# Performance work log

Hardware: AMD Instinct MI355X
Metric: run time of the kernel (lower is better)

The kernel has to match this reference:

```python
import jax, jax.numpy as jnp
import numpy as np

D = 512      # hidden_size
H = 8        # num_heads
EPS = 1e-5   # torch LayerNorm default eps


def _ln(x, g, b):
    m = x.mean(-1, keepdims=True)
    v = ((x - m) ** 2).mean(-1, keepdims=True)
    return (x - m) * jax.lax.rsqrt(v + EPS) * g + b


def _xavier(k, shape):
    fan_in, fan_out = shape
    lim = (6.0 / (fan_in + fan_out)) ** 0.5
    return jax.random.uniform(k, shape, jnp.float32, -lim, lim)


def setup_inputs() -> dict:
    key = jax.random.key(0)
    ks = jax.random.split(key, 8)
    lengths = np.array([512, 640, 768, 896, 1024, 512, 768, 1024], dtype=np.int64)
    cum = np.concatenate([np.zeros(1, np.int64), np.cumsum(lengths)])  # [9], last = 6144
    T = int(cum[-1])
    return {
        "h_n": jax.random.normal(ks[0], (T, D), jnp.float32),
        "to_v_w": _xavier(ks[1], (D, D)), "to_v_b": jnp.zeros((D,), jnp.float32),
        "to_qk_w": _xavier(ks[2], (D, 2 * D)), "to_qk_b": jnp.zeros((2 * D,), jnp.float32),
        "proj_w": _xavier(ks[3], (D, D)), "proj_b": jnp.zeros((D,), jnp.float32),
        "ffn_w1": _xavier(ks[4], (D, 4 * D)), "ffn_b1": jnp.zeros((4 * D,), jnp.float32),
        "ffn_w2": _xavier(ks[5], (4 * D, D)), "ffn_b2": jnp.zeros((D,), jnp.float32),
        "ln1_g": jnp.ones((D,), jnp.float32), "ln1_b": jnp.zeros((D,), jnp.float32),
        "ln2_g": jnp.ones((D,), jnp.float32), "ln2_b": jnp.zeros((D,), jnp.float32),
        "num_query_cumsum": jnp.asarray(cum),
    }


def reference(h_n, to_v_w, to_v_b, to_qk_w, to_qk_b, proj_w, proj_b,
              ffn_w1, ffn_b1, ffn_w2, ffn_b2, ln1_g, ln1_b, ln2_g, ln2_b,
              num_query_cumsum):
    # --- static ragged layout (indices are constants) ---
    cum = np.asarray(num_query_cumsum)
    lengths = np.diff(cum)                       # [B]
    B = int(lengths.size)
    N = int(lengths.max())                       # max_num_nodes
    T = int(cum[-1])
    bid = np.repeat(np.arange(B), lengths)       # [T] graph id per token
    pos = np.arange(T) - cum[bid]                # [T] slot within graph
    pad_mask = np.arange(N)[None, :] >= lengths[:, None]  # [B, N], True = padding

    hd = D // H
    scale = hd ** -0.5

    # --- projections on the flat ragged tokens ---
    v = h_n @ to_v_w + to_v_b                    # [T, D]
    qk = h_n @ to_qk_w + to_qk_b                 # [T, 2D]
    q, k = qk[:, :D], qk[:, D:]

    # --- pad ragged -> dense [B, H, N, hd] ---
    def pad(x):
        xp = jnp.zeros((B, N, D), x.dtype).at[bid, pos].set(x)
        return xp.reshape(B, N, H, hd).transpose(0, 2, 1, 3)

    qp, kp, vp = pad(q), pad(k), pad(v)

    # --- dense masked softmax attention (keys masked at pad slots) ---
    scores = jnp.einsum('bhnd,bhmd->bhnm', qp, kp) * scale
    scores = jnp.where(pad_mask[:, None, None, :], -jnp.inf, scores)
    attn = jax.nn.softmax(scores, axis=-1)
    ctx = jnp.einsum('bhnm,bhmd->bhnd', attn, vp)

    # --- unpad back to flat [T, D] ---
    h_new = ctx.transpose(0, 2, 1, 3).reshape(B, N, D)[bid, pos]

    # --- residual + LN + FFN + LN (dropout = 0) ---
    h1 = _ln(h_n + (h_new @ proj_w + proj_b), ln1_g, ln1_b)
    ffn = jax.nn.gelu(h1 @ ffn_w1 + ffn_b1, approximate=False) @ ffn_w2 + ffn_b2
    return _ln(h1 + ffn, ln2_g, ln2_b)
```

## Files before the change

### kernel.cpp

```cpp
#include <hip/hip_runtime.h>

typedef __bf16 bf16;
typedef __bf16 bf16x8 __attribute__((ext_vector_type(8)));
typedef __bf16 bf16x4 __attribute__((ext_vector_type(4)));
typedef float  f32x4  __attribute__((ext_vector_type(4)));

#define MFMA16 __builtin_amdgcn_mfma_f32_16x16x32_bf16

__device__ __forceinline__ void gl2lds16(const bf16* g, bf16* l) {
  __builtin_amdgcn_global_load_lds(
      (const __attribute__((address_space(1))) unsigned int*)g,
      (__attribute__((address_space(3))) unsigned int*)l, 16, 0, 0);
}

__device__ __forceinline__ int dt_bf16(const void* g1) {
  return (((const unsigned*)g1)[0] == 0x3F800000u) ? 0 : 1;
}
__device__ __forceinline__ float load_any(const void* p, int i, int f) {
  return f ? (float)((const bf16*)p)[i] : ((const float*)p)[i];
}

__device__ __forceinline__ float gelu_fast(float x) {
  const float u = 0.7978845608028654f * (x + 0.044715f * x * x * x);
  const float e = __builtin_amdgcn_exp2f(2.8853900817779268f * u);
  return x * e * __builtin_amdgcn_rcpf(e + 1.0f);
}

__global__ __launch_bounds__(256) void prep_all(
    const void* __restrict__ h, const void* __restrict__ w_qk,
    const void* __restrict__ w_v, const void* __restrict__ w_pr,
    const void* __restrict__ w_f1, const void* __restrict__ w_f2,
    const void* __restrict__ b_qk, const void* __restrict__ b_v,
    const void* __restrict__ b_pr, const void* __restrict__ b_f1,
    const void* __restrict__ b_f2, const void* __restrict__ g1,
    const void* __restrict__ b1, const void* __restrict__ g2,
    const void* __restrict__ b2,
    bf16* __restrict__ hb, bf16* __restrict__ Wtqkv, bf16* __restrict__ Wtpr,
    bf16* __restrict__ Wtf1, bf16* __restrict__ Wtf2,
    float* __restrict__ vec, int T) {
  __shared__ bf16 tile[32][33];
  const int f = dt_bf16(g1);
  const int t = threadIdx.x;
  int b = blockIdx.x;
  const int HB = (T * 512) / 2048;

  if (b < HB) {
    const int i = (b * 256 + t) * 8;
    if (f) {
      *(bf16x8*)&hb[i] = *(const bf16x8*)((const bf16*)h + i);
    } else {
      const float* hf = (const float*)h;
      bf16x8 v;
#pragma unroll
      for (int j = 0; j < 8; j++) v[j] = (bf16)hf[i + j];
      *(bf16x8*)&hb[i] = v;
    }
    return;
  }
  b -= HB;

  if (b < 3072) {
    const void* in; bf16* out; int K, N;
    if (b < 512)       { in = w_qk; out = Wtqkv;                     K = 512;  N = 1024; }
    else if (b < 768)  { b -= 512;  in = w_v;  out = Wtqkv + (size_t)1024 * 512; K = 512; N = 512; }
    else if (b < 1024) { b -= 768;  in = w_pr; out = Wtpr;           K = 512;  N = 512; }
    else if (b < 2048) { b -= 1024; in = w_f1; out = Wtf1;           K = 512;  N = 2048; }
    else               { b -= 2048; in = w_f2; out = Wtf2;           K = 2048; N = 512; }
    const int tilesx = N / 32;
    const int bx = (b % tilesx) * 32, by = (b / tilesx) * 32;
    const int tx = t & 31, ty = t >> 5;
#pragma unroll
    for (int i = 0; i < 32; i += 8)
      tile[ty + i][tx] = (bf16)load_any(in, (by + ty + i) * N + bx + tx, f);
    __syncthreads();
#pragma unroll
    for (int i = 0; i < 32; i += 8)
      out[(size_t)(bx + ty + i) * K + by + tx] = tile[tx][ty + i];
    return;
  }
  b -= 3072;

  const int i = b * 256 + t;
  if (i >= 6656) return;
  const void* src; int base;
  if (i < 1024)      { src = b_qk; base = 0; }
  else if (i < 1536) { src = b_v;  base = 1024; }
  else if (i < 2048) { src = b_pr; base = 1536; }
  else if (i < 4096) { src = b_f1; base = 2048; }
  else if (i < 4608) { src = b_f2; base = 4096; }
  else if (i < 5120) { src = g1;   base = 4608; }
  else if (i < 5632) { src = b1;   base = 5120; }
  else if (i < 6144) { src = g2;   base = 5632; }
  else               { src = b2;   base = 6144; }
  vec[i] = load_any(src, i - base, f);
}

template <int BM, int BN, int WM, int WN, int MODE>
__global__ __launch_bounds__(256) void gemm_lds(const bf16* __restrict__ A,
                                                const bf16* __restrict__ Bt,
                                                const float* __restrict__ bias,
                                                void* __restrict__ aux,
                                                void* __restrict__ outp,
                                                int N, int K, int ldA, int ldB,
                                                int ldT) {
  constexpr int WAVES_M = BM / WM;
  constexpr int WAVES_N = BN / WN;
  static_assert(WAVES_M * WAVES_N == 4, "4 waves per block");
  constexpr int MI = WM / 16;
  constexpr int NI = WN / 16;
  __shared__ __align__(16) bf16 As[BM * 64];
  __shared__ __align__(16) bf16 Bs[BN * 64];
  const int t = threadIdx.x;
  const int m0 = blockIdx.x * BM, n0 = blockIdx.y * BN;
  const int lane = t & 63, wv = t >> 6;
  const int wm = (wv / WAVES_N) * WM;
  const int wn = (wv % WAVES_N) * WN;
  const int qd = lane >> 4, cl = lane & 15;

  const f32x4 fz = {0.f, 0.f, 0.f, 0.f};
  f32x4 acc[MI][NI];
#pragma unroll
  for (int i = 0; i < MI; i++)
#pragma unroll
    for (int j = 0; j < NI; j++) acc[i][j] = fz;

  const int srow = wv * 8 + (lane >> 3);
  const int sch = (lane & 7) ^ (lane >> 3);
  const bf16* pA = A + (size_t)(m0 + srow) * ldA + sch * 8;
  const bf16* pB = Bt + (size_t)(n0 + srow) * ldB + sch * 8;
  bf16* AsW = As + wv * 8 * 64;
  bf16* BsW = Bs + wv * 8 * 64;

  for (int k0 = 0; k0 < K; k0 += 64) {
    __syncthreads();
#pragma unroll
    for (int op = 0; op < BM / 32; op++)
      gl2lds16(pA + (size_t)(op * 32) * ldA, AsW + op * 32 * 64);
#pragma unroll
    for (int op = 0; op < BN / 32; op++)
      gl2lds16(pB + (size_t)(op * 32) * ldB, BsW + op * 32 * 64);
    pA += 64; pB += 64;
    __syncthreads();

#pragma unroll
    for (int ss = 0; ss < 2; ss++) {
      bf16x8 af[MI], bfr[NI];
#pragma unroll
      for (int i = 0; i < MI; i++)
        af[i] = *(const bf16x8*)&As[(wm + i * 16 + cl) * 64 +
                                    ((ss * 4 + qd) ^ (cl & 7)) * 8];
#pragma unroll
      for (int i = 0; i < NI; i++)
        bfr[i] = *(const bf16x8*)&Bs[(wn + i * 16 + cl) * 64 +
                                     ((ss * 4 + qd) ^ (cl & 7)) * 8];
#pragma unroll
      for (int mi = 0; mi < MI; mi++)
#pragma unroll
        for (int ni = 0; ni < NI; ni++)
          acc[mi][ni] = MFMA16(af[mi], bfr[ni], acc[mi][ni], 0, 0, 0);
    }
  }

  float bv[NI];
#pragma unroll
  for (int ni = 0; ni < NI; ni++) bv[ni] = bias[n0 + wn + ni * 16 + cl];

#pragma unroll
  for (int mi = 0; mi < MI; mi++) {
    const int mbase = m0 + wm + mi * 16 + qd * 4;
#pragma unroll
    for (int ni = 0; ni < NI; ni++) {
      const int n = n0 + wn + ni * 16 + cl;
      if (MODE == 5) {
        if (n0 < 1024) {
          bf16* out = (bf16*)outp;
#pragma unroll
          for (int r = 0; r < 4; r++)
            out[(size_t)(mbase + r) * 1024 + n] = (bf16)(acc[mi][ni][r] + bv[ni]);
        } else {
          bf16* vtp = (bf16*)aux;
          bf16x4 pk;
#pragma unroll
          for (int r = 0; r < 4; r++) pk[r] = (bf16)(acc[mi][ni][r] + bv[ni]);
          *(bf16x4*)&vtp[(size_t)(n - 1024) * ldT + mbase] = pk;
        }
      } else if (MODE == 2) {
        float* out = (float*)outp;
        const bf16* res = (const bf16*)aux;
#pragma unroll
        for (int r = 0; r < 4; r++)
          out[(size_t)(mbase + r) * N + n] =
              acc[mi][ni][r] + bv[ni] + (float)res[(size_t)(mbase + r) * N + n];
      } else {
        bf16* out = (bf16*)outp;
#pragma unroll
        for (int r = 0; r < 4; r++)
          out[(size_t)(mbase + r) * N + n] = (bf16)gelu_fast(acc[mi][ni][r] + bv[ni]);
      }
    }
  }
}

__global__ __launch_bounds__(256) void attn_kernel(const bf16* __restrict__ qk,
                                                   const bf16* __restrict__ vt,
                                                   bf16* __restrict__ ctx,
                                                   const int* __restrict__ cumraw,
                                                   int T, int ncum) {
  __shared__ __align__(16) bf16 Ks[2][64 * 64];
  __shared__ __align__(16) bf16 Vs[2][64 * 64];
  __shared__ __align__(16) bf16 P[4][16 * 64];
  const int wv = threadIdx.x >> 6, lane = threadIdx.x & 63;
  const int qd = lane >> 4, cl = lane & 15;
  const int q0b = blockIdx.x * 64;
  const int q0 = q0b + wv * 16;
  const int h = blockIdx.y;

  const int stride = (cumraw[1] == 0) ? 2 : 1;
  int kstart = 0, kend = T;
  for (int i = 1; i < ncum; i++) {
    int c = cumraw[i * stride];
    if (c > q0b) { kend = c; break; }
    kstart = c;
  }

  const bf16* qbase = qk + (size_t)(q0 + cl) * 1024 + h * 64 + qd * 8;
  bf16x8 qf0 = *(const bf16x8*)qbase;
  bf16x8 qf1 = *(const bf16x8*)(qbase + 32);

  const f32x4 fz = {0.f, 0.f, 0.f, 0.f};
  f32x4 o[4] = {fz, fz, fz, fz};
  float lacc[4] = {0.f, 0.f, 0.f, 0.f};

  const int srow = wv * 8 + (lane >> 3);
  const int schunk = (lane & 7) ^ (srow & 7);
  const bf16* kg = qk + 512 + (size_t)h * 64 + schunk * 8;
  const bf16* vg = vt + (size_t)(h * 64 + srow) * T + schunk * 8;
  const int woff = wv * 8 * 64;

  const int bch = qd ^ (cl & 7);
  const float cc = 0.1803368801111204f;

  {
    const bf16* kg0 = kg + (size_t)(kstart + srow) * 1024;
    gl2lds16(kg0, Ks[0] + woff);
    gl2lds16(kg0 + (size_t)32 * 1024, Ks[0] + woff + 32 * 64);
    const bf16* vg0 = vg + kstart;
    gl2lds16(vg0, Vs[0] + woff);
    gl2lds16(vg0 + (size_t)32 * T, Vs[0] + woff + 32 * 64);
  }

  int ib = 0;
  for (int kc = kstart; kc < kend; kc += 64, ib ^= 1) {
    __syncthreads();

    if (kc + 64 < kend) {
      const bf16* kg0 = kg + (size_t)(kc + 64 + srow) * 1024;
      gl2lds16(kg0, Ks[ib ^ 1] + woff);
      gl2lds16(kg0 + (size_t)32 * 1024, Ks[ib ^ 1] + woff + 32 * 64);
      const bf16* vg0 = vg + kc + 64;
      gl2lds16(vg0, Vs[ib ^ 1] + woff);
      gl2lds16(vg0 + (size_t)32 * T, Vs[ib ^ 1] + woff + 32 * 64);
    }

    f32x4 s[4];
#pragma unroll
    for (int ni = 0; ni < 4; ni++) {
      const bf16* kr = Ks[ib] + (ni * 16 + cl) * 64;
      f32x4 tacc = fz;
      tacc = MFMA16(qf0, *(const bf16x8*)(kr + bch * 8), tacc, 0, 0, 0);
      tacc = MFMA16(qf1, *(const bf16x8*)(kr + (bch ^ 4) * 8), tacc, 0, 0, 0);
      s[ni] = tacc;
    }

    bf16* Pw = P[wv];
#pragma unroll
    for (int r = 0; r < 4; r++) {
      const float p0 = __builtin_amdgcn_exp2f(s[0][r] * cc);
      const float p1 = __builtin_amdgcn_exp2f(s[1][r] * cc);
      const float p2 = __builtin_amdgcn_exp2f(s[2][r] * cc);
      const float p3 = __builtin_amdgcn_exp2f(s[3][r] * cc);
      lacc[r] += (p0 + p1) + (p2 + p3);
      const int prow = qd * 4 + r;
      const int px = prow & 7;
      const int cb = cl >> 3, ci = cl & 7;
      Pw[prow * 64 + ((cb ^ px) * 8) + ci] = (bf16)p0;
      Pw[prow * 64 + (((2 + cb) ^ px) * 8) + ci] = (bf16)p1;
      Pw[prow * 64 + (((4 + cb) ^ px) * 8) + ci] = (bf16)p2;
      Pw[prow * 64 + (((6 + cb) ^ px) * 8) + ci] = (bf16)p3;
    }

    const int pch = qd ^ (cl & 7);
    const bf16* pr = Pw + cl * 64;
    bf16x8 pf0 = *(const bf16x8*)(pr + pch * 8);
    bf16x8 pf1 = *(const bf16x8*)(pr + (pch ^ 4) * 8);
#pragma unroll
    for (int dt = 0; dt < 4; dt++) {
      const bf16* vr = Vs[ib] + (dt * 16 + cl) * 64;
      o[dt] = MFMA16(pf0, *(const bf16x8*)(vr + bch * 8), o[dt], 0, 0, 0);
      o[dt] = MFMA16(pf1, *(const bf16x8*)(vr + (bch ^ 4) * 8), o[dt], 0, 0, 0);
    }
  }

  float linv[4];
#pragma unroll
  for (int r = 0; r < 4; r++) {
    float l = lacc[r];
    l += __shfl_xor(l, 1);
    l += __shfl_xor(l, 2);
    l += __shfl_xor(l, 4);
    l += __shfl_xor(l, 8);
    linv[r] = __builtin_amdgcn_rcpf(l);
  }
#pragma unroll
  for (int dt = 0; dt < 4; dt++) {
#pragma unroll
    for (int r = 0; r < 4; r++) {
      float y = o[dt][r] * linv[r];
      ctx[(size_t)(q0 + qd * 4 + r) * 512 + h * 64 + dt * 16 + cl] = (bf16)y;
    }
  }
}

__global__ __launch_bounds__(256) void ln_kernel(const float* __restrict__ s,
                                                 const float* __restrict__ g,
                                                 const float* __restrict__ b,
                                                 bf16* __restrict__ outb) {
  const int row = blockIdx.x * 4 + (threadIdx.x >> 6);
  const int lane = threadIdx.x & 63;
  const float4* sr = (const float4*)(s + (size_t)row * 512);
  float4 x0 = sr[lane];
  float4 x1 = sr[lane + 64];
  float sum = x0.x + x0.y + x0.z + x0.w + x1.x + x1.y + x1.z + x1.w;
  float sq = x0.x * x0.x + x0.y * x0.y + x0.z * x0.z + x0.w * x0.w +
             x1.x * x1.x + x1.y * x1.y + x1.z * x1.z + x1.w * x1.w;
#pragma unroll
  for (int off = 1; off < 64; off <<= 1) {
    sum += __shfl_xor(sum, off);
    sq += __shfl_xor(sq, off);
  }
  const float mean = sum * (1.0f / 512.0f);
  const float var = sq * (1.0f / 512.0f) - mean * mean;
  const float rs = rsqrtf(var + 1e-5f);
  const float4* gp = (const float4*)g;
  const float4* bp = (const float4*)b;
  float4 g0 = gp[lane], g1v = gp[lane + 64];
  float4 b0 = bp[lane], b1v = bp[lane + 64];
  float xv[8] = {x0.x, x0.y, x0.z, x0.w, x1.x, x1.y, x1.z, x1.w};
  float gv[8] = {g0.x, g0.y, g0.z, g0.w, g1v.x, g1v.y, g1v.z, g1v.w};
  float bb[8] = {b0.x, b0.y, b0.z, b0.w, b1v.x, b1v.y, b1v.z, b1v.w};
  bf16x4 o0, o1;
#pragma unroll
  for (int j = 0; j < 4; j++) {
    o0[j] = (bf16)((xv[j] - mean) * rs * gv[j] + bb[j]);
    o1[j] = (bf16)((xv[4 + j] - mean) * rs * gv[4 + j] + bb[4 + j]);
  }
  *(bf16x4*)&outb[(size_t)row * 512 + lane * 4] = o0;
  *(bf16x4*)&outb[(size_t)row * 512 + 256 + lane * 4] = o1;
}

__global__ __launch_bounds__(256) void ln2_kernel(const float* __restrict__ s,
                                                  const float* __restrict__ g,
                                                  const float* __restrict__ b,
                                                  void* __restrict__ outb,
                                                  const void* __restrict__ g1probe) {
  const int row = blockIdx.x * 4 + (threadIdx.x >> 6);
  const int lane = threadIdx.x & 63;
  const float4* sr = (const float4*)(s + (size_t)row * 512);
  float4 x0 = sr[lane];
  float4 x1 = sr[lane + 64];
  float sum = x0.x + x0.y + x0.z + x0.w + x1.x + x1.y + x1.z + x1.w;
  float sq = x0.x * x0.x + x0.y * x0.y + x0.z * x0.z + x0.w * x0.w +
             x1.x * x1.x + x1.y * x1.y + x1.z * x1.z + x1.w * x1.w;
#pragma unroll
  for (int off = 1; off < 64; off <<= 1) {
    sum += __shfl_xor(sum, off);
    sq += __shfl_xor(sq, off);
  }
  const float mean = sum * (1.0f / 512.0f);
  const float var = sq * (1.0f / 512.0f) - mean * mean;
  const float rs = rsqrtf(var + 1e-5f);
  const float4* gp = (const float4*)g;
  const float4* bp = (const float4*)b;
  float4 g0 = gp[lane], g1v = gp[lane + 64];
  float4 b0 = bp[lane], b1v = bp[lane + 64];
  float xv[8] = {x0.x, x0.y, x0.z, x0.w, x1.x, x1.y, x1.z, x1.w};
  float gv[8] = {g0.x, g0.y, g0.z, g0.w, g1v.x, g1v.y, g1v.z, g1v.w};
  float bb[8] = {b0.x, b0.y, b0.z, b0.w, b1v.x, b1v.y, b1v.z, b1v.w};
  float y[8];
#pragma unroll
  for (int j = 0; j < 8; j++) y[j] = (xv[j] - mean) * rs * gv[j] + bb[j];

  if (dt_bf16(g1probe)) {
    bf16* ob = (bf16*)outb;
    bf16x4 o0, o1;
#pragma unroll
    for (int j = 0; j < 4; j++) { o0[j] = (bf16)y[j]; o1[j] = (bf16)y[4 + j]; }
    *(bf16x4*)&ob[(size_t)row * 512 + lane * 4] = o0;
    *(bf16x4*)&ob[(size_t)row * 512 + 256 + lane * 4] = o1;
  } else {
    float4* of = (float4*)((float*)outb + (size_t)row * 512);
    of[lane] = make_float4(y[0], y[1], y[2], y[3]);
    of[lane + 64] = make_float4(y[4], y[5], y[6], y[7]);
  }
}

extern "C" void kernel_launch(void* const* d_in, const int* in_sizes, int n_in,
                              void* d_out, int out_size, void* d_ws, size_t ws_size,
                              hipStream_t stream) {
  (void)n_in; (void)out_size; (void)ws_size;
  const void* h_n  = d_in[0];
  const void* w_v  = d_in[1];
  const void* b_v  = d_in[2];
  const void* w_qk = d_in[3];
  const void* b_qk = d_in[4];
  const void* w_pr = d_in[5];
  const void* b_pr = d_in[6];
  const void* w_f1 = d_in[7];
  const void* b_f1 = d_in[8];
  const void* w_f2 = d_in[9];
  const void* b_f2 = d_in[10];
  const void* g1w  = d_in[11];
  const void* b1w  = d_in[12];
  const void* g2w  = d_in[13];
  const void* b2w  = d_in[14];
  const int* cum   = (const int*)d_in[15];
  const int T = in_sizes[0] / 512;
  const int ncum = in_sizes[15];

  char* ws = (char*)d_ws;
  size_t off = 0;
  auto alloc = [&](size_t bytes) {
    char* p = ws + off;
    off += (bytes + 255) & ~(size_t)255;
    return p;
  };
  float* vec = (float*)alloc(6656 * 4);
  bf16* hb   = (bf16*)alloc((size_t)T * 512 * 2);
  bf16* qkb  = (bf16*)alloc((size_t)T * 1024 * 2);
  bf16* vt   = (bf16*)alloc((size_t)T * 512 * 2);
  bf16* ctx  = (bf16*)alloc((size_t)T * 512 * 2);
  float* s1  = (float*)alloc((size_t)T * 512 * 4);
  bf16* h1b  = (bf16*)alloc((size_t)T * 512 * 2);
  bf16* Wtqkv = (bf16*)alloc((size_t)1536 * 512 * 2);
  bf16* Wtpr  = (bf16*)alloc((size_t)512 * 512 * 2);
  bf16* Wtf1  = (bf16*)alloc((size_t)2048 * 512 * 2);
  bf16* Wtf2  = (bf16*)alloc((size_t)512 * 2048 * 2);
  bf16* gbuf = qkb;
  float* s2 = s1;

  float* fb_qkv = vec + 0;
  float* fb_pr  = vec + 1536;
  float* fb_f1  = vec + 2048;
  float* fb_f2  = vec + 4096;
  float* fg1 = vec + 4608, *fb1 = vec + 5120;
  float* fg2 = vec + 5632, *fb2 = vec + 6144;

  const int prep_blocks = (T * 512) / 2048 + 3072 + 26;
  prep_all<<<prep_blocks, 256, 0, stream>>>(
      h_n, w_qk, w_v, w_pr, w_f1, w_f2,
      b_qk, b_v, b_pr, b_f1, b_f2, g1w, b1w, g2w, b2w,
      hb, Wtqkv, Wtpr, Wtf1, Wtf2, vec, T);

  gemm_lds<64, 128, 32, 64, 5><<<dim3(T / 64, 12), 256, 0, stream>>>(
      hb, Wtqkv, fb_qkv, vt, qkb, 1536, 512, 512, 512, T);
  attn_kernel<<<dim3(T / 64, 8), 256, 0, stream>>>(qkb, vt, ctx, cum, T, ncum);
  gemm_lds<32, 128, 16, 64, 2><<<dim3(T / 32, 4), 256, 0, stream>>>(
      ctx, Wtpr, fb_pr, (void*)hb, s1, 512, 512, 512, 512, 0);
  ln_kernel<<<T / 4, 256, 0, stream>>>(s1, fg1, fb1, h1b);
  gemm_lds<128, 128, 64, 64, 3><<<dim3(T / 128, 16), 256, 0, stream>>>(
      h1b, Wtf1, fb_f1, nullptr, gbuf, 2048, 512, 512, 512, 0);
  gemm_lds<32, 128, 16, 64, 2><<<dim3(T / 32, 4), 256, 0, stream>>>(
      gbuf, Wtf2, fb_f2, (void*)h1b, s2, 512, 2048, 2048, 2048, 0);
  ln2_kernel<<<T / 4, 256, 0, stream>>>(s2, fg2, fb2, d_out, g1w);
}
```

Baseline: 211.3 us.

## Split attention keys across two blocks and merge partial results

Splits each query tile's key range into two halves handled by separate blocks (grid z=2). Each block writes unnormalized bf16 partial outputs and row sums, and a new merge kernel adds them and normalizes. This doubles the number of attention blocks to improve occupancy over the 256 CUs. The K/V double-buffered prefetch is replaced with single-buffered synchronous loads, which adds an extra kernel launch and exposes load latency. The softmax uses no running max, so plain summation of the partials is consistent, but rounding each partial to bf16 adds precision loss.

```diff
diff --git a/kernel.cpp b/kernel.cpp
--- a/kernel.cpp
+++ b/kernel.cpp
@@ -203,17 +203,19 @@
 
 __global__ __launch_bounds__(256) void attn_kernel(const bf16* __restrict__ qk,
                                                    const bf16* __restrict__ vt,
-                                                   bf16* __restrict__ ctx,
+                                                   bf16* __restrict__ opart,
+                                                   float* __restrict__ lpart,
                                                    const int* __restrict__ cumraw,
                                                    int T, int ncum) {
-  __shared__ __align__(16) bf16 Ks[2][64 * 64];
-  __shared__ __align__(16) bf16 Vs[2][64 * 64];
+  __shared__ __align__(16) bf16 Ks[64 * 64];
+  __shared__ __align__(16) bf16 Vs[64 * 64];
   __shared__ __align__(16) bf16 P[4][16 * 64];
   const int wv = threadIdx.x >> 6, lane = threadIdx.x & 63;
   const int qd = lane >> 4, cl = lane & 15;
   const int q0b = blockIdx.x * 64;
   const int q0 = q0b + wv * 16;
   const int h = blockIdx.y;
+  const int z = blockIdx.z;
 
   const int stride = (cumraw[1] == 0) ? 2 : 1;
   int kstart = 0, kend = T;
@@ -222,6 +224,11 @@
     if (c > q0b) { kend = c; break; }
     kstart = c;
   }
+  const int steps = (kend - kstart) >> 6;
+  const int half = ((steps + 1) >> 1) << 6;
+  const int ks_z = kstart + (z ? half : 0);
+  int ke_z = z ? kend : (kstart + half);
+  if (ke_z > kend) ke_z = kend;
 
   const bf16* qbase = qk + (size_t)(q0 + cl) * 1024 + h * 64 + qd * 8;
   bf16x8 qf0 = *(const bf16x8*)qbase;
@@ -240,32 +247,20 @@
   const int bch = qd ^ (cl & 7);
   const float cc = 0.1803368801111204f;
 
-  {
-    const bf16* kg0 = kg + (size_t)(kstart + srow) * 1024;
-    gl2lds16(kg0, Ks[0] + woff);
-    gl2lds16(kg0 + (size_t)32 * 1024, Ks[0] + woff + 32 * 64);
-    const bf16* vg0 = vg + kstart;
-    gl2lds16(vg0, Vs[0] + woff);
-    gl2lds16(vg0 + (size_t)32 * T, Vs[0] + woff + 32 * 64);
-  }
-
-  int ib = 0;
-  for (int kc = kstart; kc < kend; kc += 64, ib ^= 1) {
+  for (int kc = ks_z; kc < ke_z; kc += 64) {
     __syncthreads();
-
-    if (kc + 64 < kend) {
-      const bf16* kg0 = kg + (size_t)(kc + 64 + srow) * 1024;
-      gl2lds16(kg0, Ks[ib ^ 1] + woff);
-      gl2lds16(kg0 + (size_t)32 * 1024, Ks[ib ^ 1] + woff + 32 * 64);
-      const bf16* vg0 = vg + kc + 64;
-      gl2lds16(vg0, Vs[ib ^ 1] + woff);
-      gl2lds16(vg0 + (size_t)32 * T, Vs[ib ^ 1] + woff + 32 * 64);
-    }
+    const bf16* kg0 = kg + (size_t)(kc + srow) * 1024;
+    gl2lds16(kg0, Ks + woff);
+    gl2lds16(kg0 + (size_t)32 * 1024, Ks + woff + 32 * 64);
+    const bf16* vg0 = vg + kc;
+    gl2lds16(vg0, Vs + woff);
+    gl2lds16(vg0 + (size_t)32 * T, Vs + woff + 32 * 64);
+    __syncthreads();
 
     f32x4 s[4];
 #pragma unroll
     for (int ni = 0; ni < 4; ni++) {
-      const bf16* kr = Ks[ib] + (ni * 16 + cl) * 64;
+      const bf16* kr = Ks + (ni * 16 + cl) * 64;
       f32x4 tacc = fz;
       tacc = MFMA16(qf0, *(const bf16x8*)(kr + bch * 8), tacc, 0, 0, 0);
       tacc = MFMA16(qf1, *(const bf16x8*)(kr + (bch ^ 4) * 8), tacc, 0, 0, 0);
@@ -295,13 +290,12 @@
     bf16x8 pf1 = *(const bf16x8*)(pr + (pch ^ 4) * 8);
 #pragma unroll
     for (int dt = 0; dt < 4; dt++) {
-      const bf16* vr = Vs[ib] + (dt * 16 + cl) * 64;
+      const bf16* vr = Vs + (dt * 16 + cl) * 64;
       o[dt] = MFMA16(pf0, *(const bf16x8*)(vr + bch * 8), o[dt], 0, 0, 0);
       o[dt] = MFMA16(pf1, *(const bf16x8*)(vr + (bch ^ 4) * 8), o[dt], 0, 0, 0);
     }
   }
 
-  float linv[4];
 #pragma unroll
   for (int r = 0; r < 4; r++) {
     float l = lacc[r];
@@ -309,16 +303,34 @@
     l += __shfl_xor(l, 2);
     l += __shfl_xor(l, 4);
     l += __shfl_xor(l, 8);
-    linv[r] = __builtin_amdgcn_rcpf(l);
-  }
+    if (cl == 0)
+      lpart[((size_t)z * T + q0 + qd * 4 + r) * 8 + h] = l;
+  }
+  const size_t obase = (size_t)z * T * 512;
 #pragma unroll
   for (int dt = 0; dt < 4; dt++) {
 #pragma unroll
     for (int r = 0; r < 4; r++) {
-      float y = o[dt][r] * linv[r];
-      ctx[(size_t)(q0 + qd * 4 + r) * 512 + h * 64 + dt * 16 + cl] = (bf16)y;
-    }
-  }
+      opart[obase + (size_t)(q0 + qd * 4 + r) * 512 + h * 64 + dt * 16 + cl] =
+          (bf16)o[dt][r];
+    }
+  }
+}
+
+__global__ __launch_bounds__(256) void attn_merge(const bf16* __restrict__ opart,
+                                                  const float* __restrict__ lpart,
+                                                  bf16* __restrict__ ctx, int T) {
+  const int row = blockIdx.x * 4 + (threadIdx.x >> 6);
+  const int lane = threadIdx.x & 63;
+  const int h = lane >> 3;
+  bf16x8 a = *(const bf16x8*)&opart[(size_t)row * 512 + lane * 8];
+  bf16x8 b = *(const bf16x8*)&opart[(size_t)(T + row) * 512 + lane * 8];
+  const float l = lpart[(size_t)row * 8 + h] + lpart[((size_t)T + row) * 8 + h];
+  const float li = __builtin_amdgcn_rcpf(l);
+  bf16x8 o;
+#pragma unroll
+  for (int j = 0; j < 8; j++) o[j] = (bf16)(((float)a[j] + (float)b[j]) * li);
+  *(bf16x8*)&ctx[(size_t)row * 512 + lane * 8] = o;
 }
 
 __global__ __launch_bounds__(256) void ln_kernel(const float* __restrict__ s,
@@ -441,6 +453,8 @@
   bf16* ctx  = (bf16*)alloc((size_t)T * 512 * 2);
   float* s1  = (float*)alloc((size_t)T * 512 * 4);
   bf16* h1b  = (bf16*)alloc((size_t)T * 512 * 2);
+  bf16* opart = (bf16*)alloc((size_t)2 * T * 512 * 2);
+  float* lpart = (float*)alloc((size_t)2 * T * 8 * 4);
   bf16* Wtqkv = (bf16*)alloc((size_t)1536 * 512 * 2);
   bf16* Wtpr  = (bf16*)alloc((size_t)512 * 512 * 2);
   bf16* Wtf1  = (bf16*)alloc((size_t)2048 * 512 * 2);
@@ -463,7 +477,9 @@
 
   gemm_lds<64, 128, 32, 64, 5><<<dim3(T / 64, 12), 256, 0, stream>>>(
       hb, Wtqkv, fb_qkv, vt, qkb, 1536, 512, 512, 512, T);
-  attn_kernel<<<dim3(T / 64, 8), 256, 0, stream>>>(qkb, vt, ctx, cum, T, ncum);
+  attn_kernel<<<dim3(T / 64, 8, 2), 256, 0, stream>>>(qkb, vt, opart, lpart,
+                                                      cum, T, ncum);
+  attn_merge<<<T / 4, 256, 0, stream>>>(opart, lpart, ctx, T);
   gemm_lds<32, 128, 16, 64, 2><<<dim3(T / 32, 4), 256, 0, stream>>>(
       ctx, Wtpr, fb_pr, (void*)hb, s1, 512, 512, 512, 512, 0);
   ln_kernel<<<T / 4, 256, 0, stream>>>(s1, fg1, fb1, h1b);
```

Result: slower. 217.1 us (+2.8%).

## Split-K the FFN down-projection into two partial sums reduced in LN2

Applied to the files above, without the earlier changes.

The FFN2 GEMM (K=2048) now runs as a split-K launch with two z-slices over K=1024 each, using 64x128 tiles instead of 32x128. Each slice writes an fp32 partial to a new buffer, with bias and residual added only by slice 0. The final layernorm kernel reads both partials and sums them before normalizing. This is meant to cut the long per-block K loop and raise parallelism, at the cost of extra fp32 write and read traffic and more workspace.

```diff
diff --git a/kernel.cpp b/kernel.cpp
--- a/kernel.cpp
+++ b/kernel.cpp
@@ -116,6 +116,7 @@
   const int wm = (wv / WAVES_N) * WM;
   const int wn = (wv % WAVES_N) * WN;
   const int qd = lane >> 4, cl = lane & 15;
+  const int koff = (MODE == 6) ? blockIdx.z * K : 0;
 
   const f32x4 fz = {0.f, 0.f, 0.f, 0.f};
   f32x4 acc[MI][NI];
@@ -126,8 +127,8 @@
 
   const int srow = wv * 8 + (lane >> 3);
   const int sch = (lane & 7) ^ (lane >> 3);
-  const bf16* pA = A + (size_t)(m0 + srow) * ldA + sch * 8;
-  const bf16* pB = Bt + (size_t)(n0 + srow) * ldB + sch * 8;
+  const bf16* pA = A + (size_t)(m0 + srow) * ldA + koff + sch * 8;
+  const bf16* pB = Bt + (size_t)(n0 + srow) * ldB + koff + sch * 8;
   bf16* AsW = As + wv * 8 * 64;
   bf16* BsW = Bs + wv * 8 * 64;
 
@@ -191,11 +192,21 @@
         for (int r = 0; r < 4; r++)
           out[(size_t)(mbase + r) * N + n] =
               acc[mi][ni][r] + bv[ni] + (float)res[(size_t)(mbase + r) * N + n];
-      } else {
+      } else if (MODE == 3) {
         bf16* out = (bf16*)outp;
 #pragma unroll
         for (int r = 0; r < 4; r++)
           out[(size_t)(mbase + r) * N + n] = (bf16)gelu_fast(acc[mi][ni][r] + bv[ni]);
+      } else {
+        float* out = (float*)outp + (size_t)blockIdx.z * ldT;
+        const bf16* res = (const bf16*)aux;
+#pragma unroll
+        for (int r = 0; r < 4; r++) {
+          float v = acc[mi][ni][r];
+          if (blockIdx.z == 0)
+            v += bv[ni] + (float)res[(size_t)(mbase + r) * N + n];
+          out[(size_t)(mbase + r) * N + n] = v;
+        }
       }
     }
   }
@@ -358,19 +369,27 @@
   *(bf16x4*)&outb[(size_t)row * 512 + 256 + lane * 4] = o1;
 }
 
-__global__ __launch_bounds__(256) void ln2_kernel(const float* __restrict__ s,
+__global__ __launch_bounds__(256) void ln2_kernel(const float* __restrict__ sa,
+                                                  const float* __restrict__ sb,
                                                   const float* __restrict__ g,
                                                   const float* __restrict__ b,
                                                   void* __restrict__ outb,
                                                   const void* __restrict__ g1probe) {
   const int row = blockIdx.x * 4 + (threadIdx.x >> 6);
   const int lane = threadIdx.x & 63;
-  const float4* sr = (const float4*)(s + (size_t)row * 512);
-  float4 x0 = sr[lane];
-  float4 x1 = sr[lane + 64];
-  float sum = x0.x + x0.y + x0.z + x0.w + x1.x + x1.y + x1.z + x1.w;
-  float sq = x0.x * x0.x + x0.y * x0.y + x0.z * x0.z + x0.w * x0.w +
-             x1.x * x1.x + x1.y * x1.y + x1.z * x1.z + x1.w * x1.w;
+  const float4* pa = (const float4*)(sa + (size_t)row * 512);
+  const float4* pb = (const float4*)(sb + (size_t)row * 512);
+  float4 a0 = pa[lane], a1 = pa[lane + 64];
+  float4 c0 = pb[lane], c1 = pb[lane + 64];
+  float x[8];
+#pragma unroll
+  for (int j = 0; j < 4; j++) {
+    x[j] = (&a0.x)[j] + (&c0.x)[j];
+    x[4 + j] = (&a1.x)[j] + (&c1.x)[j];
+  }
+  float sum = 0.f, sq = 0.f;
+#pragma unroll
+  for (int j = 0; j < 8; j++) { sum += x[j]; sq += x[j] * x[j]; }
 #pragma unroll
   for (int off = 1; off < 64; off <<= 1) {
     sum += __shfl_xor(sum, off);
@@ -383,12 +402,11 @@
   const float4* bp = (const float4*)b;
   float4 g0 = gp[lane], g1v = gp[lane + 64];
   float4 b0 = bp[lane], b1v = bp[lane + 64];
-  float xv[8] = {x0.x, x0.y, x0.z, x0.w, x1.x, x1.y, x1.z, x1.w};
   float gv[8] = {g0.x, g0.y, g0.z, g0.w, g1v.x, g1v.y, g1v.z, g1v.w};
   float bb[8] = {b0.x, b0.y, b0.z, b0.w, b1v.x, b1v.y, b1v.z, b1v.w};
   float y[8];
 #pragma unroll
-  for (int j = 0; j < 8; j++) y[j] = (xv[j] - mean) * rs * gv[j] + bb[j];
+  for (int j = 0; j < 8; j++) y[j] = (x[j] - mean) * rs * gv[j] + bb[j];
 
   if (dt_bf16(g1probe)) {
     bf16* ob = (bf16*)outb;
@@ -441,12 +459,12 @@
   bf16* ctx  = (bf16*)alloc((size_t)T * 512 * 2);
   float* s1  = (float*)alloc((size_t)T * 512 * 4);
   bf16* h1b  = (bf16*)alloc((size_t)T * 512 * 2);
+  float* s2p = (float*)alloc((size_t)2 * T * 512 * 4);
   bf16* Wtqkv = (bf16*)alloc((size_t)1536 * 512 * 2);
   bf16* Wtpr  = (bf16*)alloc((size_t)512 * 512 * 2);
   bf16* Wtf1  = (bf16*)alloc((size_t)2048 * 512 * 2);
   bf16* Wtf2  = (bf16*)alloc((size_t)512 * 2048 * 2);
   bf16* gbuf = qkb;
-  float* s2 = s1;
 
   float* fb_qkv = vec + 0;
   float* fb_pr  = vec + 1536;
@@ -469,7 +487,8 @@
   ln_kernel<<<T / 4, 256, 0, stream>>>(s1, fg1, fb1, h1b);
   gemm_lds<128, 128, 64, 64, 3><<<dim3(T / 128, 16), 256, 0, stream>>>(
       h1b, Wtf1, fb_f1, nullptr, gbuf, 2048, 512, 512, 512, 0);
-  gemm_lds<32, 128, 16, 64, 2><<<dim3(T / 32, 4), 256, 0, stream>>>(
-      gbuf, Wtf2, fb_f2, (void*)h1b, s2, 512, 2048, 2048, 2048, 0);
-  ln2_kernel<<<T / 4, 256, 0, stream>>>(s2, fg2, fb2, d_out, g1w);
-}
+  gemm_lds<64, 128, 32, 64, 6><<<dim3(T / 64, 4, 2), 256, 0, stream>>>(
+      gbuf, Wtf2, fb_f2, (void*)h1b, s2p, 512, 1024, 2048, 2048, T * 512);
+  ln2_kernel<<<T / 4, 256, 0, stream>>>(s2p, s2p + (size_t)T * 512, fg2, fb2,
+                                        d_out, g1w);
+}
```

Result: no change. 211.6 us (+0.2%).
